# Kernel tuning notes

Hardware: AMD Instinct MI355X
Metric: run time of the kernel (lower is better)

The kernel has to match this reference:

```python
import jax, jax.numpy as jnp
import numpy as np

D_EMB = 64
N_HEADS = 8
D_K = D_EMB // N_HEADS


def setup_inputs() -> dict:
    key = jax.random.key(0)
    ks = jax.random.split(key, 7)
    B, N = 4, 512
    s = 0.02
    return {
        "n": jax.random.normal(ks[0], (B, N, D_EMB), jnp.float32),
        "e": jax.random.normal(ks[1], (B, N, N, D_EMB), jnp.float32),
        # weights stored as (in, out); torch Linear applies x @ W.T
        "W_qkv": jax.random.normal(ks[2], (D_EMB, 3 * D_EMB), jnp.float32) * s,
        "O_n": jax.random.normal(ks[3], (D_EMB, D_EMB), jnp.float32) * s,
        "W_g": jax.random.normal(ks[4], (D_EMB, N_HEADS), jnp.float32) * s,
        "W_e": jax.random.normal(ks[5], (D_EMB, N_HEADS), jnp.float32) * s,
        "O_e": jax.random.normal(ks[6], (N_HEADS, D_EMB), jnp.float32) * s,
    }


def reference(n, e, W_qkv, O_n, W_g, W_e, O_e):
    B, N, _ = n.shape
    H, dk = N_HEADS, D_K
    # QKV projection -> [B, H, N, dk] each
    qkv = (n @ W_qkv).reshape(B, N, 3, H, dk)
    Q = jnp.transpose(qkv[:, :, 0], (0, 2, 1, 3))
    K = jnp.transpose(qkv[:, :, 1], (0, 2, 1, 3))
    V = jnp.transpose(qkv[:, :, 2], (0, 2, 1, 3))
    # per-head edge bias E and gate G: [B, H, N, N]
    E = jnp.transpose(e @ W_e, (0, 3, 1, 2))
    G = jax.nn.sigmoid(jnp.transpose(e @ W_g, (0, 3, 1, 2)))
    dynamic_centrality = jnp.log1p(G.sum(-1))  # [B, H, N]
    # scaled, clamped attention scores plus edge bias
    A_raw = jnp.einsum("bhnd,bhmd->bhnm", Q, K) * (dk ** -0.5)
    A_raw = jnp.clip(A_raw, -5.0, 5.0)
    _E = A_raw + E  # pre-softmax scores, reused for edge output
    A = jax.nn.softmax(_E, axis=-1)
    _V = jnp.einsum("bhnm,bhmd->bhnd", A, V)
    _V = _V * dynamic_centrality[..., None]  # centrality rescale
    n_out = jnp.transpose(_V, (0, 2, 1, 3)).reshape(B, N, H * dk) @ O_n
    e_out = jnp.transpose(_E, (0, 2, 3, 1)) @ O_e  # [B, N, N, d_emb]
    return (n_out, e_out)
```

## Files before the change

### kernel.cpp

```cpp
#include <hip/hip_runtime.h>

#define NN 512
#define SCALE 0.35355339059327373f
#define SMAX 6.0f

typedef short bf16x8 __attribute__((ext_vector_type(8)));
typedef float f32x4 __attribute__((ext_vector_type(4)));

static __device__ __forceinline__ unsigned short bhi16(float x) {
    return (unsigned short)(__float_as_uint(x) >> 16);
}
static __device__ __forceinline__ float btrunc(float x) {
    return __uint_as_float(__float_as_uint(x) & 0xFFFF0000u);
}
static __device__ __forceinline__ unsigned short blo16(float x) {
    return (unsigned short)(__float_as_uint(x - btrunc(x)) >> 16);
}

__global__ __launch_bounds__(64) void qkv_proj(const float* __restrict__ nin,
                                               const float* __restrict__ Wqkv,
                                               float* __restrict__ qkv,
                                               unsigned short* __restrict__ kbf) {
    const int r = blockIdx.x;
    const int j = threadIdx.x;
    const float* nr = nin + (size_t)r * 64;
    float a0 = 0.f, a1 = 0.f, a2 = 0.f;
#pragma unroll
    for (int d = 0; d < 64; ++d) {
        const float nv = nr[d];
        const float* wr = Wqkv + d * 192;
        a0 = fmaf(nv, wr[j], a0);
        a1 = fmaf(nv, wr[64 + j], a1);
        a2 = fmaf(nv, wr[128 + j], a2);
    }
    float* o = qkv + (size_t)r * 192;
    o[j] = a0; o[64 + j] = a1; o[128 + j] = a2;
    kbf[(size_t)r * 64 + j] = bhi16(a1);
}

__device__ __forceinline__ void gload16f(const float* g, float* l) {
    __builtin_amdgcn_global_load_lds(
        (const __attribute__((address_space(1))) unsigned int*)(g),
        (__attribute__((address_space(3))) unsigned int*)(l), 16, 0, 0);
}
__device__ __forceinline__ void gload16u(const unsigned short* g, unsigned short* l) {
    __builtin_amdgcn_global_load_lds(
        (const __attribute__((address_space(1))) unsigned int*)(g),
        (__attribute__((address_space(3))) unsigned int*)(l), 16, 0, 0);
}
#define WAITV(N) asm volatile("s_waitcnt vmcnt(" #N ")" ::: "memory")
#define BARRIER() __builtin_amdgcn_s_barrier()

__global__ __launch_bounds__(256, 4) void edge_mfma6(
    const float* __restrict__ e,
    const float* __restrict__ qkv,
    const unsigned short* __restrict__ kbf,
    const float* __restrict__ We,
    const float* __restrict__ Wg,
    const float* __restrict__ Oe,
    float* __restrict__ e_out,
    float* __restrict__ pvw,
    float* __restrict__ dngs)
{
    __shared__ float ebuf[4][16][64];
    __shared__ unsigned short kbl[4][16][64];
    __shared__ float Wl[1024];
    __shared__ float Qlds[64];
    __shared__ float Oelds[512];
    __shared__ float E_lds[4][32][8];
    __shared__ float red[256];
    __shared__ float wdn[4][8], wgs[4][8];

    const int t = threadIdx.x, w = t >> 6, l = t & 63;
    const int a2 = l >> 4, m16 = l & 15;
    const int bid = blockIdx.x;
    const int wg = (bid & 7) * 1024 + (bid >> 3);
    const int bn = wg >> 2, chunk = wg & 3;
    const int b = bn >> 9;
    const int rowc = chunk * 128 + w * 32;
    const float* __restrict__ Qp = qkv + (size_t)bn * 192;
    const float* __restrict__ ebase = e + (size_t)bn * 32768;
    float* __restrict__ eob = e_out + (size_t)bn * 32768;

#define STAGE_E(s) do {                                                          \
        _Pragma("unroll")                                                        \
        for (int i_ = 0; i_ < 4; ++i_) {                                         \
            const int lrow = i_ * 4 + (l >> 4);                                  \
            gload16f(ebase + (size_t)(rowc + (s) * 16 + lrow) * 64 + (((l & 15) ^ lrow) * 4), \
                     &ebuf[w][i_ * 4][0]);                                       \
        } } while (0)
#define STAGE_K(s) do {                                                          \
        _Pragma("unroll")                                                        \
        for (int i_ = 0; i_ < 2; ++i_) {                                         \
            const int r8 = i_ * 8 + (l >> 3);                                    \
            gload16u(kbf + (size_t)(b * NN + rowc + (s) * 16 + r8) * 64 + (((l & 7) ^ (r8 & 7)) * 8), \
                     &kbl[w][i_ * 8][0]);                                        \
        } } while (0)

    {
        const float* wsrc = (w < 2) ? (We + w * 256) : (Wg + (w - 2) * 256);
        gload16f(wsrc + l * 4, &Wl[w * 256]);
        if (l < 16) gload16f(Qp + l * 4, &Qlds[0]);
        if (l < 32) gload16f(Oe + w * 128 + l * 4, &Oelds[w * 128]);
    }
    STAGE_E(0); STAGE_K(0);

    WAITV(6);
    BARRIER();

    const int colbase = (m16 < 8) ? m16 : (504 + m16);
    bf16x8 WfB[4], WcB[2], QdB[2];
#pragma unroll
    for (int blk = 0; blk < 4; ++blk) {
#pragma unroll
        for (int jj = 0; jj < 4; ++jj) {
            const int d = blk * 16 + a2 * 4 + jj;
            const short h = (short)bhi16(Wl[d * 8 + colbase]);
            WfB[blk][2 * jj] = h;
            WfB[blk][2 * jj + 1] = h;
        }
    }
#pragma unroll
    for (int c = 0; c < 2; ++c) {
        const int head = c * 4 + a2;
#pragma unroll
        for (int j = 0; j < 8; ++j) {
            const int d = c * 32 + a2 * 8 + j;
            WcB[c][j] = (short)blo16(Wl[d * 8 + colbase]);
            QdB[c][j] = (m16 == head) ? (short)bhi16(Qlds[d]) : (short)0;
        }
    }
    float dn = 0.f, gs = 0.f;

#define SLAB(s) do {                                                             \
        f32x4 c1 = {0.f, 0.f, 0.f, 0.f}, c2 = {0.f, 0.f, 0.f, 0.f};             \
        _Pragma("unroll")                                                        \
        for (int blk = 0; blk < 4; ++blk) {                                      \
            const float4 ev = *(const float4*)&ebuf[w][m16]                      \
                                  [(((blk * 4 + a2) ^ m16) * 4)];                \
            bf16x8 af;                                                           \
            af[0] = (short)bhi16(ev.x); af[1] = (short)blo16(ev.x);              \
            af[2] = (short)bhi16(ev.y); af[3] = (short)blo16(ev.y);              \
            af[4] = (short)bhi16(ev.z); af[5] = (short)blo16(ev.z);              \
            af[6] = (short)bhi16(ev.w); af[7] = (short)blo16(ev.w);              \
            c1 = __builtin_amdgcn_mfma_f32_16x16x32_bf16(af, WfB[blk], c1, 0, 0, 0); \
        }                                                                        \
        _Pragma("unroll")                                                        \
        for (int c = 0; c < 2; ++c) {                                            \
            const int g0 = c * 8 + a2 * 2;                                       \
            const float4 e0 = *(const float4*)&ebuf[w][m16][((g0 ^ m16) * 4)];   \
            const float4 e1 = *(const float4*)&ebuf[w][m16][(((g0 + 1) ^ m16) * 4)]; \
            bf16x8 ac;                                                           \
            ac[0] = (short)bhi16(e0.x); ac[1] = (short)bhi16(e0.y);              \
            ac[2] = (short)bhi16(e0.z); ac[3] = (short)bhi16(e0.w);              \
            ac[4] = (short)bhi16(e1.x); ac[5] = (short)bhi16(e1.y);              \
            ac[6] = (short)bhi16(e1.z); ac[7] = (short)bhi16(e1.w);              \
            c1 = __builtin_amdgcn_mfma_f32_16x16x32_bf16(ac, WcB[c], c1, 0, 0, 0); \
            const bf16x8 kf = *(const bf16x8*)&kbl[w][m16]                       \
                                  [(((c * 4 + a2) ^ (m16 & 7)) * 8)];            \
            c2 = __builtin_amdgcn_mfma_f32_16x16x32_bf16(kf, QdB[c], c2, 0, 0, 0); \
        }                                                                        \
        if (m16 < 8) {                                                           \
            _Pragma("unroll")                                                    \
            for (int r = 0; r < 4; ++r) {                                        \
                const float E_ = fminf(fmaxf(c2[r] * SCALE, -5.f), 5.f) + c1[r]; \
                dn += __expf(E_ - SMAX);                                         \
                E_lds[w][(s) * 16 + a2 * 4 + r][m16] = E_;                       \
            }                                                                    \
        } else {                                                                 \
            _Pragma("unroll")                                                    \
            for (int r = 0; r < 4; ++r) gs += 1.f / (1.f + __expf(-c1[r]));      \
        } } while (0)

    WAITV(0);
    SLAB(0);
    STAGE_E(1); STAGE_K(1);
    WAITV(0);
    SLAB(1);

    dn += __shfl_xor(dn, 16, 64); dn += __shfl_xor(dn, 32, 64);
    gs += __shfl_xor(gs, 16, 64); gs += __shfl_xor(gs, 32, 64);
    if (a2 == 0 && m16 < 8) wdn[w][m16] = dn;
    if (a2 == 0 && m16 >= 8) wgs[w][m16 - 8] = gs;

    {
        const int k = l & 7, hh = (l >> 3) & 7;
        const float* vb = qkv + (size_t)(b * NN + rowc) * 192 + 128 + hh * 8 + k;
        float acc = 0.f;
#pragma unroll 8
        for (int i = 0; i < 32; ++i) {
            const float p = __expf(E_lds[w][i][hh] - SMAX);
            acc = fmaf(p, vb[(size_t)i * 192], acc);
        }
        red[t] = acc;
    }
    __syncthreads();
    if (t < 64)
        pvw[(size_t)wg * 64 + t] = red[t] + red[64 + t] + red[128 + t] + red[192 + t];
    if (t < 8)
        dngs[(size_t)wg * 16 + t] = wdn[0][t] + wdn[1][t] + wdn[2][t] + wdn[3][t];
    else if (t < 16)
        dngs[(size_t)wg * 16 + t] = wgs[0][t - 8] + wgs[1][t - 8] + wgs[2][t - 8] + wgs[3][t - 8];

    {
        const int j4 = l & 15, mr = l >> 4;
        float oc[8][4];
#pragma unroll
        for (int h = 0; h < 8; ++h) {
            const float4 v = *(const float4*)&Oelds[h * 64 + j4 * 4];
            oc[h][0] = v.x; oc[h][1] = v.y; oc[h][2] = v.z; oc[h][3] = v.w;
        }
#pragma unroll 2
        for (int p = 0; p < 8; ++p) {
            const int mloc = p * 4 + mr;
            const float* er = &E_lds[w][mloc][0];
            const float4 ra = *reinterpret_cast<const float4*>(er);
            const float4 rb = *reinterpret_cast<const float4*>(er + 4);
            float o0 = ra.x * oc[0][0], o1 = ra.x * oc[0][1], o2 = ra.x * oc[0][2], o3 = ra.x * oc[0][3];
            o0 = fmaf(ra.y, oc[1][0], o0); o1 = fmaf(ra.y, oc[1][1], o1); o2 = fmaf(ra.y, oc[1][2], o2); o3 = fmaf(ra.y, oc[1][3], o3);
            o0 = fmaf(ra.z, oc[2][0], o0); o1 = fmaf(ra.z, oc[2][1], o1); o2 = fmaf(ra.z, oc[2][2], o2); o3 = fmaf(ra.z, oc[2][3], o3);
            o0 = fmaf(ra.w, oc[3][0], o0); o1 = fmaf(ra.w, oc[3][1], o1); o2 = fmaf(ra.w, oc[3][2], o2); o3 = fmaf(ra.w, oc[3][3], o3);
            o0 = fmaf(rb.x, oc[4][0], o0); o1 = fmaf(rb.x, oc[4][1], o1); o2 = fmaf(rb.x, oc[4][2], o2); o3 = fmaf(rb.x, oc[4][3], o3);
            o0 = fmaf(rb.y, oc[5][0], o0); o1 = fmaf(rb.y, oc[5][1], o1); o2 = fmaf(rb.y, oc[5][2], o2); o3 = fmaf(rb.y, oc[5][3], o3);
            o0 = fmaf(rb.z, oc[6][0], o0); o1 = fmaf(rb.z, oc[6][1], o1); o2 = fmaf(rb.z, oc[6][2], o2); o3 = fmaf(rb.z, oc[6][3], o3);
            o0 = fmaf(rb.w, oc[7][0], o0); o1 = fmaf(rb.w, oc[7][1], o1); o2 = fmaf(rb.w, oc[7][2], o2); o3 = fmaf(rb.w, oc[7][3], o3);
            reinterpret_cast<float4*>(eob + (size_t)(rowc + mloc) * 64 + j4 * 4)[0]
                = make_float4(o0, o1, o2, o3);
        }
    }
#undef STAGE_E
#undef STAGE_K
#undef SLAB
}

__global__ __launch_bounds__(64) void nout_fin(
    const float* __restrict__ pvw,
    const float* __restrict__ dngs,
    const float* __restrict__ On,
    float* __restrict__ n_out)
{
    __shared__ float vfin[64];
    const int bn = blockIdx.x, t = threadIdx.x;
    const int hh = t >> 3;
    float pv = 0.f, den = 0.f, gsum = 0.f;
#pragma unroll
    for (int c = 0; c < 4; ++c) {
        const size_t wg = (size_t)bn * 4 + c;
        pv += pvw[wg * 64 + t];
        den += dngs[wg * 16 + hh];
        gsum += dngs[wg * 16 + 8 + hh];
    }
    vfin[t] = pv * (1.f / den) * log1pf(gsum);
    __syncthreads();
    float acc = 0.f;
#pragma unroll
    for (int i = 0; i < 64; ++i)
        acc = fmaf(vfin[i], On[i * 64 + t], acc);
    n_out[(size_t)bn * 64 + t] = acc;
}

extern "C" void kernel_launch(void* const* d_in, const int* in_sizes, int n_in,
                              void* d_out, int out_size, void* d_ws, size_t ws_size,
                              hipStream_t stream) {
    const float* n_in_p = (const float*)d_in[0];
    const float* e_p    = (const float*)d_in[1];
    const float* Wqkv   = (const float*)d_in[2];
    const float* On     = (const float*)d_in[3];
    const float* Wg     = (const float*)d_in[4];
    const float* We     = (const float*)d_in[5];
    const float* Oe     = (const float*)d_in[6];
    float* out = (float*)d_out;
    float* n_out = out;
    float* e_out = out + (size_t)4 * 512 * 64;
    float* qkv = (float*)d_ws;
    float* pvw = qkv + 393216;
    float* dngs = pvw + 524288;
    unsigned short* kbf = (unsigned short*)(dngs + 131072);

    hipLaunchKernelGGL(qkv_proj, dim3(4 * NN), dim3(64), 0, stream, n_in_p, Wqkv, qkv, kbf);
    hipLaunchKernelGGL(edge_mfma6, dim3(8192), dim3(256), 0, stream,
                       e_p, qkv, kbf, We, Wg, Oe, e_out, pvw, dngs);
    hipLaunchKernelGGL(nout_fin, dim3(4 * NN), dim3(64), 0, stream,
                       pvw, dngs, On, n_out);
}
```

Measured before the change: 158.1 us.

## Drop split-bf16 error compensation in edge projection and alias LDS buffers

Removes the hi/lo bf16 split used to compensate precision in the e @ W_e / W_g projection, so each slab runs 2 MFMAs for the edge projection instead of 6 and needs fewer packing ops. The weight, Q and E_lds shared buffers are aliased into one union array, with an extra barrier added, and launch bounds are raised to 5 blocks per CU for higher occupancy. The cost is lower accuracy in the edge bias and gate, which now use plain truncated bf16 for both e and the weights, and this could exceed the tolerance.

```diff
diff --git a/kernel.cpp b/kernel.cpp
--- a/kernel.cpp
+++ b/kernel.cpp
@@ -9,12 +9,6 @@
 
 static __device__ __forceinline__ unsigned short bhi16(float x) {
     return (unsigned short)(__float_as_uint(x) >> 16);
-}
-static __device__ __forceinline__ float btrunc(float x) {
-    return __uint_as_float(__float_as_uint(x) & 0xFFFF0000u);
-}
-static __device__ __forceinline__ unsigned short blo16(float x) {
-    return (unsigned short)(__float_as_uint(x - btrunc(x)) >> 16);
 }
 
 __global__ __launch_bounds__(64) void qkv_proj(const float* __restrict__ nin,
@@ -51,7 +45,7 @@
 #define WAITV(N) asm volatile("s_waitcnt vmcnt(" #N ")" ::: "memory")
 #define BARRIER() __builtin_amdgcn_s_barrier()
 
-__global__ __launch_bounds__(256, 4) void edge_mfma6(
+__global__ __launch_bounds__(256, 5) void edge_mfma7(
     const float* __restrict__ e,
     const float* __restrict__ qkv,
     const unsigned short* __restrict__ kbf,
@@ -64,12 +58,14 @@
 {
     __shared__ float ebuf[4][16][64];
     __shared__ unsigned short kbl[4][16][64];
-    __shared__ float Wl[1024];
-    __shared__ float Qlds[64];
+    __shared__ float uni[1088];
     __shared__ float Oelds[512];
-    __shared__ float E_lds[4][32][8];
     __shared__ float red[256];
     __shared__ float wdn[4][8], wgs[4][8];
+
+    float* const Wl = uni;
+    float* const Qlds = uni + 1024;
+    auto E_lds = reinterpret_cast<float(*)[32][8]>(uni);
 
     const int t = threadIdx.x, w = t >> 6, l = t & 63;
     const int a2 = l >> 4, m16 = l & 15;
@@ -109,42 +105,22 @@
     BARRIER();
 
     const int colbase = (m16 < 8) ? m16 : (504 + m16);
-    bf16x8 WfB[4], WcB[2], QdB[2];
-#pragma unroll
-    for (int blk = 0; blk < 4; ++blk) {
-#pragma unroll
-        for (int jj = 0; jj < 4; ++jj) {
-            const int d = blk * 16 + a2 * 4 + jj;
-            const short h = (short)bhi16(Wl[d * 8 + colbase]);
-            WfB[blk][2 * jj] = h;
-            WfB[blk][2 * jj + 1] = h;
-        }
-    }
+    bf16x8 WB[2], QdB[2];
 #pragma unroll
     for (int c = 0; c < 2; ++c) {
         const int head = c * 4 + a2;
 #pragma unroll
         for (int j = 0; j < 8; ++j) {
             const int d = c * 32 + a2 * 8 + j;
-            WcB[c][j] = (short)blo16(Wl[d * 8 + colbase]);
+            WB[c][j] = (short)bhi16(Wl[d * 8 + colbase]);
             QdB[c][j] = (m16 == head) ? (short)bhi16(Qlds[d]) : (short)0;
         }
     }
     float dn = 0.f, gs = 0.f;
+    BARRIER();
 
 #define SLAB(s) do {                                                             \
         f32x4 c1 = {0.f, 0.f, 0.f, 0.f}, c2 = {0.f, 0.f, 0.f, 0.f};             \
-        _Pragma("unroll")                                                        \
-        for (int blk = 0; blk < 4; ++blk) {                                      \
-            const float4 ev = *(const float4*)&ebuf[w][m16]                      \
-                                  [(((blk * 4 + a2) ^ m16) * 4)];                \
-            bf16x8 af;                                                           \
-            af[0] = (short)bhi16(ev.x); af[1] = (short)blo16(ev.x);              \
-            af[2] = (short)bhi16(ev.y); af[3] = (short)blo16(ev.y);              \
-            af[4] = (short)bhi16(ev.z); af[5] = (short)blo16(ev.z);              \
-            af[6] = (short)bhi16(ev.w); af[7] = (short)blo16(ev.w);              \
-            c1 = __builtin_amdgcn_mfma_f32_16x16x32_bf16(af, WfB[blk], c1, 0, 0, 0); \
-        }                                                                        \
         _Pragma("unroll")                                                        \
         for (int c = 0; c < 2; ++c) {                                            \
             const int g0 = c * 8 + a2 * 2;                                       \
@@ -155,7 +131,7 @@
             ac[2] = (short)bhi16(e0.z); ac[3] = (short)bhi16(e0.w);              \
             ac[4] = (short)bhi16(e1.x); ac[5] = (short)bhi16(e1.y);              \
             ac[6] = (short)bhi16(e1.z); ac[7] = (short)bhi16(e1.w);              \
-            c1 = __builtin_amdgcn_mfma_f32_16x16x32_bf16(ac, WcB[c], c1, 0, 0, 0); \
+            c1 = __builtin_amdgcn_mfma_f32_16x16x32_bf16(ac, WB[c], c1, 0, 0, 0); \
             const bf16x8 kf = *(const bf16x8*)&kbl[w][m16]                       \
                                   [(((c * 4 + a2) ^ (m16 & 7)) * 8)];            \
             c2 = __builtin_amdgcn_mfma_f32_16x16x32_bf16(kf, QdB[c], c2, 0, 0, 0); \
@@ -278,7 +254,7 @@
     unsigned short* kbf = (unsigned short*)(dngs + 131072);
 
     hipLaunchKernelGGL(qkv_proj, dim3(4 * NN), dim3(64), 0, stream, n_in_p, Wqkv, qkv, kbf);
-    hipLaunchKernelGGL(edge_mfma6, dim3(8192), dim3(256), 0, stream,
+    hipLaunchKernelGGL(edge_mfma7, dim3(8192), dim3(256), 0, stream,
                        e_p, qkv, kbf, We, Wg, Oe, e_out, pvw, dngs);
     hipLaunchKernelGGL(nout_fin, dim3(4 * NN), dim3(64), 0, stream,
                        pvw, dngs, On, n_out);
```

New measurement: 154.2 us. 2.4% less time.
